# Performance work log

Measured on AMD Instinct MI355X. Metric: run time of the kernel, lower is better.

Reference implementation:

```python
import jax, jax.numpy as jnp
import numpy as np

# --- constants matching the torch module's default-camera / material / light setup ---
IMAGE_SIZE = 128
SCALE = 1.0
FOCAL = 12.0
R_MAT = jnp.array([[-1.0, 0.0, 0.0], [0.0, 1.0, 0.0], [0.0, 0.0, -1.0]], dtype=jnp.float32)
T_VEC = jnp.array([0.0, 0.0, 2.0 * SCALE], dtype=jnp.float32)
CAM_POS = jnp.array([0.0, 0.0, 2.0 * SCALE], dtype=jnp.float32)  # camera center in world coords
LIGHT_LOC = jnp.array([0.0, 1.0, 3.0], dtype=jnp.float32)
AMB_L, DIFF_L, SPEC_L = 0.5, 0.3, 0.2          # PointLights defaults
MAT_AMB, MAT_DIFF, MAT_SPEC = 1.0, 1.0, 0.6    # Materials(specular_color=0.6)
SHININESS = 10.0
TEXEL = jnp.array([142.0, 179.0, 247.0], dtype=jnp.float32) / 255.0  # uniform vertex color
BG = 1.0  # BlendParams background
EPS = 1e-8


def _normalize(v):
    return v / (jnp.linalg.norm(v, axis=-1, keepdims=True) + EPS)


def _render_one(verts, faces):
    """verts: [V,3] world space; faces: [F,3] int. Returns ([3,H,W] rgb*255, [1,H,W] alpha)."""
    H = W = IMAGE_SIZE
    # world -> view (PyTorch3D row-vector convention: x_view = x @ R + T)
    view = verts @ R_MAT + T_VEC              # [V,3]
    z = view[:, 2]                            # [V] view-space depth (>0 in front)
    ndc = FOCAL * view[:, :2] / z[:, None]    # [V,2] perspective projection to NDC
    tri = ndc[faces]                          # [F,3,2]
    tz = z[faces]                             # [F,3]

    # pixel centers in NDC (PyTorch3D: +x left, +y up)
    xs = 1.0 - (2.0 * jnp.arange(W) + 1.0) / W
    ys = 1.0 - (2.0 * jnp.arange(H) + 1.0) / H
    gy, gx = jnp.meshgrid(ys, xs, indexing='ij')
    px = gx.reshape(-1).astype(jnp.float32)   # [P]
    py = gy.reshape(-1).astype(jnp.float32)   # [P]

    v0, v1, v2 = tri[:, 0], tri[:, 1], tri[:, 2]   # [F,2]

    def edge(a, b):  # signed area cross(b-a, p-a) for all pixels -> [P,F]
        return ((b[:, 0] - a[:, 0])[None] * (py[:, None] - a[:, 1][None])
                - (b[:, 1] - a[:, 1])[None] * (px[:, None] - a[:, 0][None]))

    area = ((v1[:, 0] - v0[:, 0]) * (v2[:, 1] - v0[:, 1])
            - (v1[:, 1] - v0[:, 1]) * (v2[:, 0] - v0[:, 0]))   # [F]
    area_safe = jnp.where(jnp.abs(area) < EPS, EPS, area)
    b0 = edge(v1, v2) / area_safe             # [P,F]
    b1 = edge(v2, v0) / area_safe
    b2 = 1.0 - b0 - b1
    inside = (b0 >= 0) & (b1 >= 0) & (b2 >= 0) & (jnp.abs(area) > EPS)[None]

    # perspective-correct interpolated depth: z_pix = 1 / sum_i(b_i / z_i)
    S = b0 / tz[:, 0] + b1 / tz[:, 1] + b2 / tz[:, 2]
    depth = jnp.where(inside & (S > EPS), 1.0 / jnp.maximum(S, EPS), jnp.inf)
    fidx = jnp.argmin(depth, axis=1)          # [P] z-buffer winner (faces_per_pixel=1)
    hit = jnp.isfinite(jnp.min(depth, axis=1))

    # --- recompute barycentrics only for the winning face per pixel (cheap, [P]) ---
    f = faces[fidx]                           # [P,3]
    tv = ndc[f]                               # [P,3,2]
    tzp = z[f]                                # [P,3]
    a0, a1, a2 = tv[:, 0], tv[:, 1], tv[:, 2]

    def edge_p(a, b):
        return (b[:, 0] - a[:, 0]) * (py - a[:, 1]) - (b[:, 1] - a[:, 1]) * (px - a[:, 0])

    ar = (a1[:, 0] - a0[:, 0]) * (a2[:, 1] - a0[:, 1]) - (a1[:, 1] - a0[:, 1]) * (a2[:, 0] - a0[:, 0])
    ar = jnp.where(jnp.abs(ar) < EPS, EPS, ar)
    bb0 = edge_p(a1, a2) / ar
    bb1 = edge_p(a2, a0) / ar
    bb2 = 1.0 - bb0 - bb1
    w = jnp.stack([bb0 / tzp[:, 0], bb1 / tzp[:, 1], bb2 / tzp[:, 2]], axis=-1)
    pc = w / (jnp.sum(w, axis=-1, keepdims=True) + EPS)   # [P,3] perspective-correct barycentrics

    # --- vertex normals (world space) ---
    fv = verts[faces]                         # [F,3,3]
    fn = jnp.cross(fv[:, 1] - fv[:, 0], fv[:, 2] - fv[:, 0])  # [F,3]
    vn = (jnp.zeros_like(verts)
          .at[faces[:, 0]].add(fn)
          .at[faces[:, 1]].add(fn)
          .at[faces[:, 2]].add(fn))
    vn = _normalize(vn)

    # --- interpolate position/normal, Phong shade ---
    pos = jnp.einsum('pk,pkd->pd', pc, verts[f])   # [P,3]
    nrm = _normalize(jnp.einsum('pk,pkd->pd', pc, vn[f]))
    l = _normalize(LIGHT_LOC - pos)
    vdir = _normalize(CAM_POS - pos)
    ndl = jax.nn.relu(jnp.sum(nrm * l, axis=-1))          # [P]
    refl = 2.0 * jnp.sum(nrm * l, axis=-1, keepdims=True) * nrm - l
    spec_cos = jax.nn.relu(jnp.sum(refl * vdir, axis=-1))
    ambient = AMB_L * MAT_AMB
    diffuse = DIFF_L * MAT_DIFF * ndl
    specular = SPEC_L * MAT_SPEC * spec_cos ** SHININESS
    color = TEXEL[None] * (ambient + diffuse[:, None]) + specular[:, None]

    rgb = jnp.where(hit[:, None], color, BG)              # hard blend with white bg
    alpha = hit.astype(verts.dtype)
    img = rgb.reshape(H, W, 3).transpose(2, 0, 1) * 255.0  # [3,H,W]
    a = alpha.reshape(1, H, W)
    return img, a


def setup_inputs() -> dict:
    key = jax.random.key(0)
    k1, k2 = jax.random.split(key)
    B, V, F = 2, 1300, 2500
    vertices = jax.random.normal(k1, (B, V, 3), dtype=jnp.float32) * 0.05  # head-scale mesh near origin
    faces = jax.random.randint(k2, (F, 3), 0, V, dtype=jnp.int32)
    return {"vertices": vertices, "faces": faces}


def reference(vertices, faces):
    # ori_size == image_size, so the area-interpolation in the torch module is the identity.
    images, alphas = jax.lax.map(lambda v: _render_one(v, faces), vertices)
    return images, alphas
```

## Files before the change

### kernel.cpp

```cpp
#include <hip/hip_runtime.h>
#include <math.h>

#pragma clang fp contract(off)

#define IMG 128
#define HW (IMG * IMG)
#define NB 2
#define NV 1300
#define NF 2500
#define NFACE (NB * NF)
#define EPSF 1e-8f
#define MAXTASK 80000
#define NWAVE 4096

#define OFF_CNT 31232
#define OFF_FACE 31744
#define OFF_RECT 271744
#define OFF_TASK 351744
#define OFF_DBUF 671744

__global__ __launch_bounds__(256) void k_face(const float* __restrict__ verts,
                                              const int* __restrict__ faces,
                                              float* __restrict__ vn,
                                              float4* __restrict__ face,
                                              int4* __restrict__ rect,
                                              unsigned* __restrict__ task,
                                              int* __restrict__ cnt) {
    int i = blockIdx.x * 256 + threadIdx.x;
    int lane = threadIdx.x & 63;
    bool act = i < NFACE;
    int nb = 0;
    int cmin = 0, cmax = 0, rmin = 0, rmax = 0;
    if (act) {
        int b = (i >= NF) ? 1 : 0;
        int f = i - b * NF;
        int i0 = faces[f * 3 + 0];
        int i1 = faces[f * 3 + 1];
        int i2 = faces[f * 3 + 2];
        const float* wv = verts + (size_t)b * NV * 3;
        float v0x = wv[i0 * 3 + 0], v0y = wv[i0 * 3 + 1], v0z = wv[i0 * 3 + 2];
        float v1x = wv[i1 * 3 + 0], v1y = wv[i1 * 3 + 1], v1z = wv[i1 * 3 + 2];
        float v2x = wv[i2 * 3 + 0], v2y = wv[i2 * 3 + 1], v2z = wv[i2 * 3 + 2];
        float z0 = 2.0f - v0z, z1 = 2.0f - v1z, z2 = 2.0f - v2z;
        float p0x = (12.0f * (-v0x)) / z0, p0y = (12.0f * v0y) / z0;
        float p1x = (12.0f * (-v1x)) / z1, p1y = (12.0f * v1y) / z1;
        float p2x = (12.0f * (-v2x)) / z2, p2y = (12.0f * v2y) / z2;

        float t1 = (p1x - p0x) * (p2y - p0y);
        float t2 = (p1y - p0y) * (p2x - p0x);
        float area = t1 - t2;
        float aabs = fabsf(area);
        float area_safe = (aabs < EPSF) ? EPSF : area;

        face[i * 3 + 0] = make_float4(p2x - p1x, p2y - p1y, p1x, p1y);
        face[i * 3 + 1] = make_float4(p0x - p2x, p0y - p2y, p2x, p2y);
        face[i * 3 + 2] = make_float4(area_safe, z0, z1, z2);

        if (aabs > EPSF) {
            float minx = fminf(p0x, fminf(p1x, p2x));
            float maxx = fmaxf(p0x, fmaxf(p1x, p2x));
            float miny = fminf(p0y, fminf(p1y, p2y));
            float maxy = fmaxf(p0y, fmaxf(p1y, p2y));
            int ci0 = (int)floorf((1.0f - maxx) * 64.0f - 0.5f) - 1;
            int ci1 = (int)floorf((1.0f - minx) * 64.0f - 0.5f) + 1;
            int ri0 = (int)floorf((1.0f - maxy) * 64.0f - 0.5f) - 1;
            int ri1 = (int)floorf((1.0f - miny) * 64.0f - 0.5f) + 1;
            if (ci1 >= 0 && ci0 <= 127 && ri1 >= 0 && ri0 <= 127) {
                cmin = max(ci0, 0); cmax = min(ci1, 127);
                rmin = max(ri0, 0); rmax = min(ri1, 127);
                nb = ((rmax - rmin) >> 3) + 1;
            }
        }
        rect[i] = make_int4(cmin, cmax, rmin, rmax);

        float ax = v1x - v0x, ay = v1y - v0y, az = v1z - v0z;
        float bx = v2x - v0x, by = v2y - v0y, bz = v2z - v0z;
        float fnx = ay * bz - az * by;
        float fny = az * bx - ax * bz;
        float fnz = ax * by - ay * bx;
        float* vnb = vn + (size_t)b * NV * 3;
        atomicAdd(&vnb[i0 * 3 + 0], fnx);
        atomicAdd(&vnb[i0 * 3 + 1], fny);
        atomicAdd(&vnb[i0 * 3 + 2], fnz);
        atomicAdd(&vnb[i1 * 3 + 0], fnx);
        atomicAdd(&vnb[i1 * 3 + 1], fny);
        atomicAdd(&vnb[i1 * 3 + 2], fnz);
        atomicAdd(&vnb[i2 * 3 + 0], fnx);
        atomicAdd(&vnb[i2 * 3 + 1], fny);
        atomicAdd(&vnb[i2 * 3 + 2], fnz);
    }
    int incl = nb;
    for (int d = 1; d < 64; d <<= 1) {
        int v = __shfl_up(incl, d, 64);
        if (lane >= d) incl += v;
    }
    int wtot = __shfl(incl, 63, 64);
    int wbase = 0;
    if (lane == 0 && wtot > 0) wbase = atomicAdd(cnt, wtot);
    wbase = __shfl(wbase, 0, 64);
    int my0 = wbase + incl - nb;
    for (int k = 0; k < nb; ++k) task[my0 + k] = (unsigned)i | ((unsigned)k << 16);
}

__global__ __launch_bounds__(256) void k_raster(const float4* __restrict__ face,
                                                const int4* __restrict__ rect,
                                                const unsigned* __restrict__ task,
                                                const int* __restrict__ cnt,
                                                unsigned long long* __restrict__ dbuf) {
    int lane = threadIdx.x & 63;
    int wave = blockIdx.x * 4 + (threadIdx.x >> 6);
    int n = *cnt;
    int lr = lane >> 3, lc = lane & 7;
    for (int t = wave; t < n; t += NWAVE) {
        unsigned tk = task[t];
        int i = (int)(tk & 0xFFFFu);
        int band = (int)(tk >> 16);
        int4 rc = rect[i];
        float4 E0 = face[i * 3 + 0];
        float4 E1 = face[i * 3 + 1];
        float4 FD = face[i * 3 + 2];
        int b = (i >= NF) ? 1 : 0;
        int f = i - b * NF;
        float as = FD.x;
        int r = rc.z + (band << 3) + lr;
        bool vr = (r <= rc.w);
        float py = 1.0f - (2.0f * (float)r + 1.0f) / 128.0f;
        unsigned long long* db = dbuf + (size_t)b * HW;
        for (int cb = rc.x; cb <= rc.y; cb += 8) {
            int c = cb + lc;
            bool v = vr && (c <= rc.y);
            float px = 1.0f - (2.0f * (float)c + 1.0f) / 128.0f;
            float u1 = E0.x * (py - E0.w);
            float u2 = E0.y * (px - E0.z);
            float e0 = u1 - u2;
            float u3 = E1.x * (py - E1.w);
            float u4 = E1.y * (px - E1.z);
            float e1 = u3 - u4;
            bool ok = v && ((as > 0.0f) ? (e0 >= 0.0f && e1 >= 0.0f)
                                        : (e0 <= 0.0f && e1 <= 0.0f));
            if (__any(ok)) {
                float b0 = e0 / as;
                float b1 = e1 / as;
                float b2 = (1.0f - b0) - b1;
                float S = ((b0 / FD.y) + (b1 / FD.z)) + (b2 / FD.w);
                if (ok && b2 >= 0.0f && S > EPSF) {
                    float depth = 1.0f / fmaxf(S, EPSF);
                    unsigned long long pk =
                        ((unsigned long long)__float_as_uint(depth) << 32) | (unsigned)f;
                    atomicMin(&db[r * IMG + c], pk);
                }
            }
        }
    }
}

__global__ __launch_bounds__(256) void k_shade(const float* __restrict__ verts,
                                               const int* __restrict__ faces,
                                               const float* __restrict__ vn,
                                               const unsigned long long* __restrict__ dbuf,
                                               float* __restrict__ out) {
    int i = blockIdx.x * 256 + threadIdx.x;
    int b = i >> 14;
    int p = i & (HW - 1);
    unsigned long long pk = dbuf[i];
    unsigned dbits = (unsigned)(pk >> 32);
    bool hit = dbits < 0x7F800000u;
    float cr = 255.0f, cg = 255.0f, cb = 255.0f, alpha = 0.0f;
    if (hit) {
        alpha = 1.0f;
        int f = (int)(unsigned)(pk & 0xFFFFFFFFull);
        int row = p >> 7;
        int col = p & 127;
        float px = 1.0f - (2.0f * (float)col + 1.0f) / 128.0f;
        float py = 1.0f - (2.0f * (float)row + 1.0f) / 128.0f;
        int i0 = faces[f * 3 + 0];
        int i1 = faces[f * 3 + 1];
        int i2 = faces[f * 3 + 2];
        const float* wv = verts + (size_t)b * NV * 3;
        float v0x = wv[i0 * 3 + 0], v0y = wv[i0 * 3 + 1], v0z = wv[i0 * 3 + 2];
        float v1x = wv[i1 * 3 + 0], v1y = wv[i1 * 3 + 1], v1z = wv[i1 * 3 + 2];
        float v2x = wv[i2 * 3 + 0], v2y = wv[i2 * 3 + 1], v2z = wv[i2 * 3 + 2];
        float z0 = 2.0f - v0z, z1 = 2.0f - v1z, z2 = 2.0f - v2z;
        float a0x = (12.0f * (-v0x)) / z0, a0y = (12.0f * v0y) / z0;
        float a1x = (12.0f * (-v1x)) / z1, a1y = (12.0f * v1y) / z1;
        float a2x = (12.0f * (-v2x)) / z2, a2y = (12.0f * v2y) / z2;

        float t1 = (a1x - a0x) * (a2y - a0y);
        float t2 = (a1y - a0y) * (a2x - a0x);
        float ar = t1 - t2;
        ar = (fabsf(ar) < EPSF) ? EPSF : ar;
        float u1 = (a2x - a1x) * (py - a1y);
        float u2 = (a2y - a1y) * (px - a1x);
        float bb0 = (u1 - u2) / ar;
        float u3 = (a0x - a2x) * (py - a2y);
        float u4 = (a0y - a2y) * (px - a2x);
        float bb1 = (u3 - u4) / ar;
        float bb2 = (1.0f - bb0) - bb1;
        float w0 = bb0 / z0;
        float w1 = bb1 / z1;
        float w2 = bb2 / z2;
        float denom = ((w0 + w1) + w2) + EPSF;
        float pc0 = w0 / denom;
        float pc1 = w1 / denom;
        float pc2 = w2 / denom;

        float posx = (pc0 * v0x + pc1 * v1x) + pc2 * v2x;
        float posy = (pc0 * v0y + pc1 * v1y) + pc2 * v2y;
        float posz = (pc0 * v0z + pc1 * v1z) + pc2 * v2z;

        const float* vnb = vn + (size_t)b * NV * 3;
        float n0x = vnb[i0 * 3 + 0], n0y = vnb[i0 * 3 + 1], n0z = vnb[i0 * 3 + 2];
        float n1x = vnb[i1 * 3 + 0], n1y = vnb[i1 * 3 + 1], n1z = vnb[i1 * 3 + 2];
        float n2x = vnb[i2 * 3 + 0], n2y = vnb[i2 * 3 + 1], n2z = vnb[i2 * 3 + 2];
        float in0 = 1.0f / (sqrtf(n0x * n0x + n0y * n0y + n0z * n0z) + EPSF);
        float in1 = 1.0f / (sqrtf(n1x * n1x + n1y * n1y + n1z * n1z) + EPSF);
        float in2 = 1.0f / (sqrtf(n2x * n2x + n2y * n2y + n2z * n2z) + EPSF);
        n0x *= in0; n0y *= in0; n0z *= in0;
        n1x *= in1; n1y *= in1; n1z *= in1;
        n2x *= in2; n2y *= in2; n2z *= in2;
        float nx = (pc0 * n0x + pc1 * n1x) + pc2 * n2x;
        float ny = (pc0 * n0y + pc1 * n1y) + pc2 * n2y;
        float nz = (pc0 * n0z + pc1 * n1z) + pc2 * n2z;
        float inn = 1.0f / (sqrtf(nx * nx + ny * ny + nz * nz) + EPSF);
        nx *= inn; ny *= inn; nz *= inn;

        float lx = 0.0f - posx, ly = 1.0f - posy, lz = 3.0f - posz;
        float iln = 1.0f / (sqrtf(lx * lx + ly * ly + lz * lz) + EPSF);
        lx *= iln; ly *= iln; lz *= iln;
        float vx = 0.0f - posx, vy = 0.0f - posy, vz = 2.0f - posz;
        float ivn = 1.0f / (sqrtf(vx * vx + vy * vy + vz * vz) + EPSF);
        vx *= ivn; vy *= ivn; vz *= ivn;

        float ndl = nx * lx + ny * ly + nz * lz;
        float ndlr = fmaxf(ndl, 0.0f);
        float rx = 2.0f * ndl * nx - lx;
        float ry = 2.0f * ndl * ny - ly;
        float rz = 2.0f * ndl * nz - lz;
        float sc = fmaxf(rx * vx + ry * vy + rz * vz, 0.0f);
        float spec = 0.2f * 0.6f * powf(sc, 10.0f);
        float shade = 0.5f * 1.0f + 0.3f * 1.0f * ndlr;
        cr = ((142.0f / 255.0f) * shade + spec) * 255.0f;
        cg = ((179.0f / 255.0f) * shade + spec) * 255.0f;
        cb = ((247.0f / 255.0f) * shade + spec) * 255.0f;
    }
    float* img = out + (size_t)b * 3 * HW;
    img[0 * HW + p] = cr;
    img[1 * HW + p] = cg;
    img[2 * HW + p] = cb;
    out[(size_t)NB * 3 * HW + (size_t)b * HW + p] = alpha;
}

extern "C" void kernel_launch(void* const* d_in, const int* in_sizes, int n_in,
                              void* d_out, int out_size, void* d_ws, size_t ws_size,
                              hipStream_t stream) {
    const float* verts = (const float*)d_in[0];
    const int* faces = (const int*)d_in[1];
    char* ws = (char*)d_ws;
    float* vn = (float*)(ws + 0);
    int* cnt = (int*)(ws + OFF_CNT);
    float4* face = (float4*)(ws + OFF_FACE);
    int4* rect = (int4*)(ws + OFF_RECT);
    unsigned* task = (unsigned*)(ws + OFF_TASK);
    unsigned long long* dbuf = (unsigned long long*)(ws + OFF_DBUF);
    float* out = (float*)d_out;

    hipMemsetAsync(ws, 0, OFF_CNT + 4, stream);
    hipMemsetAsync(ws + OFF_DBUF, 0xFF, NB * HW * 8, stream);
    k_face<<<(NFACE + 255) / 256, 256, 0, stream>>>(verts, faces, vn, face, rect, task, cnt);
    k_raster<<<NWAVE / 4, 256, 0, stream>>>(face, rect, task, cnt, dbuf);
    k_shade<<<(NB * HW) / 256, 256, 0, stream>>>(verts, faces, vn, dbuf, out);
}
```

Baseline: 110.1 us.

## Replace per-face band tasks with tile-binned rasterization and per-layer depth buffers

The face kernel now bins each triangle into 8x8 pixel tiles using conservative edge tests, appending face ids to per-tile lists with atomics. The raster kernel assigns each wave a tile and a slice of that tile's list, keeping a per-pixel running minimum in registers instead of issuing 64-bit atomicMin into a global depth buffer. The shade kernel reduces 16 partial depth layers per pixel. This removes global atomic contention and the depth-buffer memset, at the cost of more bin memory, binning atomics, a 16-way reduction, and possible imbalance when tile lists are uneven.

```diff
diff --git a/kernel.cpp b/kernel.cpp
--- a/kernel.cpp
+++ b/kernel.cpp
@@ -10,69 +10,53 @@
 #define NF 2500
 #define NFACE (NB * NF)
 #define EPSF 1e-8f
-#define MAXTASK 80000
-#define NWAVE 4096
-
-#define OFF_CNT 31232
-#define OFF_FACE 31744
-#define OFF_RECT 271744
-#define OFF_TASK 351744
-#define OFF_DBUF 671744
+#define NTILE 256
+#define NBIN (NB * NTILE)
+#define MAXBIN 2500
+#define KLAY 16
+
+#define OFF_BCNT 31232
+#define OFF_FACE 33280
+#define OFF_BINS 273280
+#define OFF_DBUF 5393280
+
+#define DINIT 0x7F800000FFFFFFFFull
 
 __global__ __launch_bounds__(256) void k_face(const float* __restrict__ verts,
                                               const int* __restrict__ faces,
                                               float* __restrict__ vn,
                                               float4* __restrict__ face,
-                                              int4* __restrict__ rect,
-                                              unsigned* __restrict__ task,
-                                              int* __restrict__ cnt) {
+                                              unsigned* __restrict__ bcnt,
+                                              unsigned* __restrict__ bins) {
     int i = blockIdx.x * 256 + threadIdx.x;
-    int lane = threadIdx.x & 63;
-    bool act = i < NFACE;
-    int nb = 0;
-    int cmin = 0, cmax = 0, rmin = 0, rmax = 0;
-    if (act) {
-        int b = (i >= NF) ? 1 : 0;
-        int f = i - b * NF;
-        int i0 = faces[f * 3 + 0];
-        int i1 = faces[f * 3 + 1];
-        int i2 = faces[f * 3 + 2];
-        const float* wv = verts + (size_t)b * NV * 3;
-        float v0x = wv[i0 * 3 + 0], v0y = wv[i0 * 3 + 1], v0z = wv[i0 * 3 + 2];
-        float v1x = wv[i1 * 3 + 0], v1y = wv[i1 * 3 + 1], v1z = wv[i1 * 3 + 2];
-        float v2x = wv[i2 * 3 + 0], v2y = wv[i2 * 3 + 1], v2z = wv[i2 * 3 + 2];
-        float z0 = 2.0f - v0z, z1 = 2.0f - v1z, z2 = 2.0f - v2z;
-        float p0x = (12.0f * (-v0x)) / z0, p0y = (12.0f * v0y) / z0;
-        float p1x = (12.0f * (-v1x)) / z1, p1y = (12.0f * v1y) / z1;
-        float p2x = (12.0f * (-v2x)) / z2, p2y = (12.0f * v2y) / z2;
-
-        float t1 = (p1x - p0x) * (p2y - p0y);
-        float t2 = (p1y - p0y) * (p2x - p0x);
-        float area = t1 - t2;
-        float aabs = fabsf(area);
-        float area_safe = (aabs < EPSF) ? EPSF : area;
-
-        face[i * 3 + 0] = make_float4(p2x - p1x, p2y - p1y, p1x, p1y);
-        face[i * 3 + 1] = make_float4(p0x - p2x, p0y - p2y, p2x, p2y);
-        face[i * 3 + 2] = make_float4(area_safe, z0, z1, z2);
-
-        if (aabs > EPSF) {
-            float minx = fminf(p0x, fminf(p1x, p2x));
-            float maxx = fmaxf(p0x, fmaxf(p1x, p2x));
-            float miny = fminf(p0y, fminf(p1y, p2y));
-            float maxy = fmaxf(p0y, fmaxf(p1y, p2y));
-            int ci0 = (int)floorf((1.0f - maxx) * 64.0f - 0.5f) - 1;
-            int ci1 = (int)floorf((1.0f - minx) * 64.0f - 0.5f) + 1;
-            int ri0 = (int)floorf((1.0f - maxy) * 64.0f - 0.5f) - 1;
-            int ri1 = (int)floorf((1.0f - miny) * 64.0f - 0.5f) + 1;
-            if (ci1 >= 0 && ci0 <= 127 && ri1 >= 0 && ri0 <= 127) {
-                cmin = max(ci0, 0); cmax = min(ci1, 127);
-                rmin = max(ri0, 0); rmax = min(ri1, 127);
-                nb = ((rmax - rmin) >> 3) + 1;
-            }
-        }
-        rect[i] = make_int4(cmin, cmax, rmin, rmax);
-
+    if (i >= NFACE) return;
+    int b = (i >= NF) ? 1 : 0;
+    int f = i - b * NF;
+    int i0 = faces[f * 3 + 0];
+    int i1 = faces[f * 3 + 1];
+    int i2 = faces[f * 3 + 2];
+    const float* wv = verts + (size_t)b * NV * 3;
+    float v0x = wv[i0 * 3 + 0], v0y = wv[i0 * 3 + 1], v0z = wv[i0 * 3 + 2];
+    float v1x = wv[i1 * 3 + 0], v1y = wv[i1 * 3 + 1], v1z = wv[i1 * 3 + 2];
+    float v2x = wv[i2 * 3 + 0], v2y = wv[i2 * 3 + 1], v2z = wv[i2 * 3 + 2];
+    float z0 = 2.0f - v0z, z1 = 2.0f - v1z, z2 = 2.0f - v2z;
+    float p0x = (12.0f * (-v0x)) / z0, p0y = (12.0f * v0y) / z0;
+    float p1x = (12.0f * (-v1x)) / z1, p1y = (12.0f * v1y) / z1;
+    float p2x = (12.0f * (-v2x)) / z2, p2y = (12.0f * v2y) / z2;
+
+    float t1 = (p1x - p0x) * (p2y - p0y);
+    float t2 = (p1y - p0y) * (p2x - p0x);
+    float area = t1 - t2;
+    float aabs = fabsf(area);
+    float area_safe = (aabs < EPSF) ? EPSF : area;
+
+    float E0x = p2x - p1x, E0y = p2y - p1y, E0z = p1x, E0w = p1y;
+    float E1x = p0x - p2x, E1y = p0y - p2y, E1z = p2x, E1w = p2y;
+    face[i * 3 + 0] = make_float4(E0x, E0y, E0z, E0w);
+    face[i * 3 + 1] = make_float4(E1x, E1y, E1z, E1w);
+    face[i * 3 + 2] = make_float4(area_safe, z0, z1, z2);
+
+    {
         float ax = v1x - v0x, ay = v1y - v0y, az = v1z - v0z;
         float bx = v2x - v0x, by = v2y - v0y, bz = v2z - v0z;
         float fnx = ay * bz - az * by;
@@ -89,69 +73,102 @@
         atomicAdd(&vnb[i2 * 3 + 1], fny);
         atomicAdd(&vnb[i2 * 3 + 2], fnz);
     }
-    int incl = nb;
-    for (int d = 1; d < 64; d <<= 1) {
-        int v = __shfl_up(incl, d, 64);
-        if (lane >= d) incl += v;
-    }
-    int wtot = __shfl(incl, 63, 64);
-    int wbase = 0;
-    if (lane == 0 && wtot > 0) wbase = atomicAdd(cnt, wtot);
-    wbase = __shfl(wbase, 0, 64);
-    int my0 = wbase + incl - nb;
-    for (int k = 0; k < nb; ++k) task[my0 + k] = (unsigned)i | ((unsigned)k << 16);
+
+    if (aabs <= EPSF) return;
+
+    float minx = fminf(p0x, fminf(p1x, p2x));
+    float maxx = fmaxf(p0x, fmaxf(p1x, p2x));
+    float miny = fminf(p0y, fminf(p1y, p2y));
+    float maxy = fmaxf(p0y, fmaxf(p1y, p2y));
+    int ci0 = (int)floorf((1.0f - maxx) * 64.0f - 0.5f) - 1;
+    int ci1 = (int)floorf((1.0f - minx) * 64.0f - 0.5f) + 1;
+    int ri0 = (int)floorf((1.0f - maxy) * 64.0f - 0.5f) - 1;
+    int ri1 = (int)floorf((1.0f - miny) * 64.0f - 0.5f) + 1;
+    if (ci1 < 0 || ci0 > 127 || ri1 < 0 || ri0 > 127) return;
+    int cmin = max(ci0, 0), cmax = min(ci1, 127);
+    int rmin = max(ri0, 0), rmax = min(ri1, 127);
+
+    float s = (area_safe > 0.0f) ? 1.0f : -1.0f;
+    float mg0 = 1e-3f * (1.0f + fabsf(E0x) + fabsf(E0y));
+    float mg1 = 1e-3f * (1.0f + fabsf(E1x) + fabsf(E1y));
+    float mg2 = mg0 + mg1 + 1e-6f;
+    unsigned* bb = bins + (size_t)(b * NTILE) * MAXBIN;
+    unsigned* bc = bcnt + b * NTILE;
+    for (int tr = (rmin >> 3); tr <= (rmax >> 3); ++tr) {
+        float y_hi = 1.0f - (2.0f * (float)(tr * 8) + 1.0f) / 128.0f;
+        float y_lo = 1.0f - (2.0f * (float)(tr * 8 + 7) + 1.0f) / 128.0f;
+        float a0a = s * E0x * (y_lo - E0w), a0b = s * E0x * (y_hi - E0w);
+        float max0y = fmaxf(a0a, a0b), min0y = fminf(a0a, a0b);
+        float a1a = s * E1x * (y_lo - E1w), a1b = s * E1x * (y_hi - E1w);
+        float max1y = fmaxf(a1a, a1b), min1y = fminf(a1a, a1b);
+        for (int tc = (cmin >> 3); tc <= (cmax >> 3); ++tc) {
+            float x_hi = 1.0f - (2.0f * (float)(tc * 8) + 1.0f) / 128.0f;
+            float x_lo = 1.0f - (2.0f * (float)(tc * 8 + 7) + 1.0f) / 128.0f;
+            float b0a = -s * E0y * (x_lo - E0z), b0b = -s * E0y * (x_hi - E0z);
+            float max0x = fmaxf(b0a, b0b), min0x = fminf(b0a, b0b);
+            float b1a = -s * E1y * (x_lo - E1z), b1b = -s * E1y * (x_hi - E1z);
+            float max1x = fmaxf(b1a, b1b), min1x = fminf(b1a, b1b);
+            if (max0y + max0x < -mg0) continue;
+            if (max1y + max1x < -mg1) continue;
+            float e2max = s * area_safe - (min0y + min0x) - (min1y + min1x);
+            if (e2max < -mg2) continue;
+            unsigned slot = atomicAdd(&bc[tr * 16 + tc], 1u);
+            bb[(size_t)(tr * 16 + tc) * MAXBIN + slot] = (unsigned)f;
+        }
+    }
 }
 
 __global__ __launch_bounds__(256) void k_raster(const float4* __restrict__ face,
-                                                const int4* __restrict__ rect,
-                                                const unsigned* __restrict__ task,
-                                                const int* __restrict__ cnt,
+                                                const unsigned* __restrict__ bcnt,
+                                                const unsigned* __restrict__ bins,
                                                 unsigned long long* __restrict__ dbuf) {
+    int id = (blockIdx.x * 1021) & 2047;
+    int kq = id & 3;
+    int raw = id >> 2;
+    int b = raw & 1;
+    int tile = raw >> 1;
+    int wid = threadIdx.x >> 6;
     int lane = threadIdx.x & 63;
-    int wave = blockIdx.x * 4 + (threadIdx.x >> 6);
-    int n = *cnt;
-    int lr = lane >> 3, lc = lane & 7;
-    for (int t = wave; t < n; t += NWAVE) {
-        unsigned tk = task[t];
-        int i = (int)(tk & 0xFFFFu);
-        int band = (int)(tk >> 16);
-        int4 rc = rect[i];
+    int k = kq * 4 + wid;
+    int bin = b * NTILE + tile;
+    int cnt = (int)bcnt[bin];
+    const unsigned* bl = bins + (size_t)bin * MAXBIN;
+
+    int r = (tile >> 4) * 8 + (lane >> 3);
+    int c = (tile & 15) * 8 + (lane & 7);
+    float px = 1.0f - (2.0f * (float)c + 1.0f) / 128.0f;
+    float py = 1.0f - (2.0f * (float)r + 1.0f) / 128.0f;
+
+    unsigned long long best = DINIT;
+    for (int j = k; j < cnt; j += KLAY) {
+        int f = (int)bl[j];
+        int i = b * NF + f;
         float4 E0 = face[i * 3 + 0];
         float4 E1 = face[i * 3 + 1];
         float4 FD = face[i * 3 + 2];
-        int b = (i >= NF) ? 1 : 0;
-        int f = i - b * NF;
         float as = FD.x;
-        int r = rc.z + (band << 3) + lr;
-        bool vr = (r <= rc.w);
-        float py = 1.0f - (2.0f * (float)r + 1.0f) / 128.0f;
-        unsigned long long* db = dbuf + (size_t)b * HW;
-        for (int cb = rc.x; cb <= rc.y; cb += 8) {
-            int c = cb + lc;
-            bool v = vr && (c <= rc.y);
-            float px = 1.0f - (2.0f * (float)c + 1.0f) / 128.0f;
-            float u1 = E0.x * (py - E0.w);
-            float u2 = E0.y * (px - E0.z);
-            float e0 = u1 - u2;
-            float u3 = E1.x * (py - E1.w);
-            float u4 = E1.y * (px - E1.z);
-            float e1 = u3 - u4;
-            bool ok = v && ((as > 0.0f) ? (e0 >= 0.0f && e1 >= 0.0f)
-                                        : (e0 <= 0.0f && e1 <= 0.0f));
-            if (__any(ok)) {
-                float b0 = e0 / as;
-                float b1 = e1 / as;
-                float b2 = (1.0f - b0) - b1;
-                float S = ((b0 / FD.y) + (b1 / FD.z)) + (b2 / FD.w);
-                if (ok && b2 >= 0.0f && S > EPSF) {
-                    float depth = 1.0f / fmaxf(S, EPSF);
-                    unsigned long long pk =
-                        ((unsigned long long)__float_as_uint(depth) << 32) | (unsigned)f;
-                    atomicMin(&db[r * IMG + c], pk);
-                }
+        float u1 = E0.x * (py - E0.w);
+        float u2 = E0.y * (px - E0.z);
+        float e0 = u1 - u2;
+        float u3 = E1.x * (py - E1.w);
+        float u4 = E1.y * (px - E1.z);
+        float e1 = u3 - u4;
+        bool ok = (as > 0.0f) ? (e0 >= 0.0f && e1 >= 0.0f)
+                              : (e0 <= 0.0f && e1 <= 0.0f);
+        if (__any(ok)) {
+            float b0 = e0 / as;
+            float b1 = e1 / as;
+            float b2 = (1.0f - b0) - b1;
+            float S = ((b0 / FD.y) + (b1 / FD.z)) + (b2 / FD.w);
+            if (ok && b2 >= 0.0f && S > EPSF) {
+                float depth = 1.0f / fmaxf(S, EPSF);
+                unsigned long long pk =
+                    ((unsigned long long)__float_as_uint(depth) << 32) | (unsigned)f;
+                if (pk < best) best = pk;
             }
         }
     }
+    dbuf[(((size_t)k * NB + b) * NTILE + tile) * 64 + lane] = best;
 }
 
 __global__ __launch_bounds__(256) void k_shade(const float* __restrict__ verts,
@@ -162,15 +179,21 @@
     int i = blockIdx.x * 256 + threadIdx.x;
     int b = i >> 14;
     int p = i & (HW - 1);
-    unsigned long long pk = dbuf[i];
+    int row = p >> 7;
+    int col = p & 127;
+    int tile = (row >> 3) * 16 + (col >> 3);
+    int idx = (row & 7) * 8 + (col & 7);
+    unsigned long long pk = DINIT;
+    for (int k = 0; k < KLAY; ++k) {
+        unsigned long long v = dbuf[(((size_t)k * NB + b) * NTILE + tile) * 64 + idx];
+        if (v < pk) pk = v;
+    }
     unsigned dbits = (unsigned)(pk >> 32);
     bool hit = dbits < 0x7F800000u;
     float cr = 255.0f, cg = 255.0f, cb = 255.0f, alpha = 0.0f;
     if (hit) {
         alpha = 1.0f;
         int f = (int)(unsigned)(pk & 0xFFFFFFFFull);
-        int row = p >> 7;
-        int col = p & 127;
         float px = 1.0f - (2.0f * (float)col + 1.0f) / 128.0f;
         float py = 1.0f - (2.0f * (float)row + 1.0f) / 128.0f;
         int i0 = faces[f * 3 + 0];
@@ -257,16 +280,14 @@
     const int* faces = (const int*)d_in[1];
     char* ws = (char*)d_ws;
     float* vn = (float*)(ws + 0);
-    int* cnt = (int*)(ws + OFF_CNT);
+    unsigned* bcnt = (unsigned*)(ws + OFF_BCNT);
     float4* face = (float4*)(ws + OFF_FACE);
-    int4* rect = (int4*)(ws + OFF_RECT);
-    unsigned* task = (unsigned*)(ws + OFF_TASK);
+    unsigned* bins = (unsigned*)(ws + OFF_BINS);
     unsigned long long* dbuf = (unsigned long long*)(ws + OFF_DBUF);
     float* out = (float*)d_out;
 
-    hipMemsetAsync(ws, 0, OFF_CNT + 4, stream);
-    hipMemsetAsync(ws + OFF_DBUF, 0xFF, NB * HW * 8, stream);
-    k_face<<<(NFACE + 255) / 256, 256, 0, stream>>>(verts, faces, vn, face, rect, task, cnt);
-    k_raster<<<NWAVE / 4, 256, 0, stream>>>(face, rect, task, cnt, dbuf);
+    hipMemsetAsync(ws, 0, OFF_FACE, stream);
+    k_face<<<(NFACE + 255) / 256, 256, 0, stream>>>(verts, faces, vn, face, bcnt, bins);
+    k_raster<<<2048, 256, 0, stream>>>(face, bcnt, bins, dbuf);
     k_shade<<<(NB * HW) / 256, 256, 0, stream>>>(verts, faces, vn, dbuf, out);
 }
```

Measured after the change: 225.0 us. 2.04x slower.
